# Performance work log

Hardware: AMD Instinct MI355X
Metric: run time of the kernel (lower is better)

## Reference

```python
import jax, jax.numpy as jnp
import numpy as np

N, P, D, C = 8192, 512, 2, 4   # queries, coeff grid points, spatial dim, num coefficients
HA = 32                        # attention_net hidden
HP, CP = 32, 16                # pointswise_mlp hidden / output
HG = 256                       # green_function_net hidden


def setup_inputs() -> dict:
    key = jax.random.key(0)
    ks = jax.random.split(key, 16)
    g = lambda k, shp, s: jax.random.normal(k, shp, dtype=jnp.float32) * s
    return {
        "r": g(ks[0], (N, 2 * D), 1.0),
        "r_prime": g(ks[1], (N, 2 * D), 1.0),
        "coeff_x": g(ks[2], (P, D), 1.0),
        "coeff_y": g(ks[3], (P, C), 1.0),
        # attention_net MLP (no bias): concat(q,k)=4 -> 32 -> 32 -> 1
        "Wa1": g(ks[4], (2 * D, HA), 0.5),
        "Wa2": g(ks[5], (HA, HA), 1.0 / np.sqrt(HA)),
        "Wa3": g(ks[6], (HA, 1), 1.0 / np.sqrt(HA)),
        # pointswise_mlp: C -> 32 -> 16
        "Wp1": g(ks[7], (C, HP), 0.5), "bp1": jnp.zeros((HP,), jnp.float32),
        "Wp2": g(ks[8], (HP, CP), 1.0 / np.sqrt(HP)), "bp2": jnp.zeros((CP,), jnp.float32),
        # green_function_net: 4+4+16=24 -> 256 -> 256 -> 1 (exp at the end)
        "Wg1": g(ks[9], (2 * D + 2 * D + CP, HG), 1.0 / np.sqrt(24.0)), "bg1": jnp.zeros((HG,), jnp.float32),
        "Wg2": g(ks[10], (HG, HG), 1.0 / np.sqrt(HG)), "bg2": jnp.zeros((HG,), jnp.float32),
        "Wg3": g(ks[11], (HG, 1), 0.1 / np.sqrt(HG)), "bg3": jnp.zeros((1,), jnp.float32),
    }


def reference(r, r_prime, coeff_x, coeff_y,
              Wa1, Wa2, Wa3, Wp1, bp1, Wp2, bp2,
              Wg1, bg1, Wg2, bg2, Wg3, bg3):
    # --- CoefficientNet: pairwise MLP attention over the coefficient grid ---
    q = r[:, :D]  # (N, 2) spatial position only
    # first layer of attn MLP on concat([q, k]) split into q- and k- parts
    h = jax.nn.relu(q @ Wa1[:D][None if False else slice(None)]  # (N, HA)
                    [..., :] [..., :]  # no-op for readability
                    if False else (q @ Wa1[:D])[:, None, :] + (coeff_x @ Wa1[D:])[None, :, :])  # (N, P, HA)
    h = jax.nn.relu(h @ Wa2)                     # (N, P, HA)
    logits = (h @ Wa3)[..., 0]                   # (N, P)
    attn = jax.nn.softmax(logits, axis=-1)       # (N, P)
    attn_out = attn @ coeff_y                    # (N, C)
    c = jax.nn.relu(attn_out @ Wp1 + bp1) @ Wp2 + bp2  # (N, CP)
    # --- GreenFunctionNet ---
    x = jnp.concatenate([r, r_prime, c], axis=-1)       # (N, 24)
    g1 = jax.nn.relu(x @ Wg1 + bg1)
    g2 = jax.nn.relu(g1 @ Wg2 + bg2)
    return jnp.exp(g2 @ Wg3 + bg3)                      # (N, 1)
```

## Files before the change

### kernel.cpp

```cpp
#include <hip/hip_runtime.h>
#include <math.h>

#define N_ 8192
#define P_ 512

typedef __fp16 half8  __attribute__((ext_vector_type(8)));
typedef __fp16 half2t __attribute__((ext_vector_type(2)));
typedef float  floatx16 __attribute__((ext_vector_type(16)));

union H8 { half8 v; half2t h2[4]; };

static __device__ __forceinline__ half2t pk2(float a, float b) {
    return __builtin_amdgcn_cvt_pkrtz(a, b);
}

#define HP_OFF 17408
#define XS_OFF 21760

__global__ __launch_bounds__(512, 4) void k_fused(
    const float* __restrict__ r,
    const float* __restrict__ rp,
    const float* __restrict__ coeff_x,
    const float* __restrict__ coeff_y,
    const float* __restrict__ Wa1,
    const float* __restrict__ Wa2,
    const float* __restrict__ Wa3,
    const float* __restrict__ Wp1,
    const float* __restrict__ bp1,
    const float* __restrict__ Wp2,
    const float* __restrict__ bp2,
    const float* __restrict__ Wg1,
    const float* __restrict__ bg1,
    const float* __restrict__ Wg2,
    const float* __restrict__ bg2,
    const float* __restrict__ Wg3,
    const float* __restrict__ bg3,
    float* __restrict__ out)
{
    __shared__ __align__(16) unsigned char reg0[49152];
    __shared__ __align__(16) float4 cyS[512];
    __shared__ float sA[8][32];
    __shared__ float aoA[4][8][32];
    __shared__ float aoS[32][4];

    const int tid  = threadIdx.x;
    const int n0   = blockIdx.x * 32;
    const int lane = tid & 63;
    const int wv   = tid >> 6;
    const int j32  = lane & 31;
    const int hl   = lane >> 5;
    const int k0g  = hl * 8;

    {
        const float2 cx = ((const float2*)coeff_x)[tid];
        half2t* wrow = (half2t*)(reg0 + tid * 96);
#pragma unroll
        for (int q = 0; q < 16; ++q) {
            const float b0 = cx.x * Wa1[64 + 2*q]     + cx.y * Wa1[96 + 2*q];
            const float b1 = cx.x * Wa1[64 + 2*q + 1] + cx.y * Wa1[96 + 2*q + 1];
            wrow[q] = pk2(b0, b1);
        }
        cyS[tid] = ((const float4*)coeff_y)[tid];
    }

    H8 anh1, anh2;
    {
        const float2 rv = ((const float2*)r)[2 * (n0 + j32)];
#pragma unroll
        for (int q = 0; q < 4; ++q) {
            const int k1 = k0g + 2*q, k2 = 16 + k0g + 2*q;
            anh1.h2[q] = pk2(rv.x*Wa1[k1]   + rv.y*Wa1[32+k1],
                             rv.x*Wa1[k1+1] + rv.y*Wa1[32+k1+1]);
            anh2.h2[q] = pk2(rv.x*Wa1[k2]   + rv.y*Wa1[32+k2],
                             rv.x*Wa1[k2+1] + rv.y*Wa1[32+k2+1]);
        }
    }
    H8 af1, af2;
#pragma unroll
    for (int q = 0; q < 4; ++q) {
        af1.h2[q] = pk2(Wa2[(k0g + 2*q)     * 32 + j32],
                        Wa2[(k0g + 2*q + 1) * 32 + j32]);
        af2.h2[q] = pk2(Wa2[(16 + k0g + 2*q)     * 32 + j32],
                        Wa2[(16 + k0g + 2*q + 1) * 32 + j32]);
    }
    half2t w3h[8];
#pragma unroll
    for (int q = 0; q < 8; ++q) {
        const int r0 = ((2*q) & 3) + 8*(q >> 1) + 4*hl;
        w3h[q] = pk2(Wa3[r0], Wa3[r0 + 1]);
    }

    __syncthreads();

    const half2t zero2 = pk2(0.f, 0.f);
    float s = 0.0f, aox = 0.f, aoy = 0.f, aoz = 0.f, aow = 0.f;

#pragma unroll 2
    for (int pl = 0; pl < 64; ++pl) {
        const int ploc = wv * 64 + pl;
        const half2t* rowq = (const half2t*)(reg0 + ploc * 96) + hl * 4;

        H8 bf1, bf2;
#pragma unroll
        for (int q = 0; q < 4; ++q) {
            bf1.h2[q] = __builtin_elementwise_max(anh1.h2[q] + rowq[q],     zero2);
            bf2.h2[q] = __builtin_elementwise_max(anh2.h2[q] + rowq[8 + q], zero2);
        }

        floatx16 zc = {};
        floatx16 acc = __builtin_amdgcn_mfma_f32_32x32x16_f16(af1.v, bf1.v, zc, 0, 0, 0);
        acc = __builtin_amdgcn_mfma_f32_32x32x16_f16(af2.v, bf2.v, acc, 0, 0, 0);

        float d0, d1, d2, d3;
        {
            half2t z0 = __builtin_elementwise_max(pk2(acc[0],  acc[1]),  zero2);
            half2t z1 = __builtin_elementwise_max(pk2(acc[2],  acc[3]),  zero2);
            half2t z2 = __builtin_elementwise_max(pk2(acc[4],  acc[5]),  zero2);
            half2t z3 = __builtin_elementwise_max(pk2(acc[6],  acc[7]),  zero2);
            half2t z4 = __builtin_elementwise_max(pk2(acc[8],  acc[9]),  zero2);
            half2t z5 = __builtin_elementwise_max(pk2(acc[10], acc[11]), zero2);
            half2t z6 = __builtin_elementwise_max(pk2(acc[12], acc[13]), zero2);
            half2t z7 = __builtin_elementwise_max(pk2(acc[14], acc[15]), zero2);
            d0 = __builtin_amdgcn_fdot2(z1, w3h[1], __builtin_amdgcn_fdot2(z0, w3h[0], 0.f, false), false);
            d1 = __builtin_amdgcn_fdot2(z3, w3h[3], __builtin_amdgcn_fdot2(z2, w3h[2], 0.f, false), false);
            d2 = __builtin_amdgcn_fdot2(z5, w3h[5], __builtin_amdgcn_fdot2(z4, w3h[4], 0.f, false), false);
            d3 = __builtin_amdgcn_fdot2(z7, w3h[7], __builtin_amdgcn_fdot2(z6, w3h[6], 0.f, false), false);
        }
        float dot = (d0 + d1) + (d2 + d3);
        dot += __shfl_xor(dot, 32);

        const float e = __expf(dot);
        const float4 cyv = cyS[ploc];
        s   += e;
        aox += e * cyv.x;
        aoy += e * cyv.y;
        aoz += e * cyv.z;
        aow += e * cyv.w;
    }

    if (lane < 32) {
        sA[wv][lane]      = s;
        aoA[0][wv][lane]  = aox;
        aoA[1][wv][lane]  = aoy;
        aoA[2][wv][lane]  = aoz;
        aoA[3][wv][lane]  = aow;
    }
    __syncthreads();

    if (tid < 32) {
        float S = 0.f, A0 = 0.f, A1 = 0.f, A2 = 0.f, A3 = 0.f;
#pragma unroll
        for (int w = 0; w < 8; ++w) {
            S  += sA[w][tid];
            A0 += aoA[0][w][tid];
            A1 += aoA[1][w][tid];
            A2 += aoA[2][w][tid];
            A3 += aoA[3][w][tid];
        }
        const float inv = 1.0f / S;
        aoS[tid][0] = A0 * inv;
        aoS[tid][1] = A1 * inv;
        aoS[tid][2] = A2 * inv;
        aoS[tid][3] = A3 * inv;
    }
    __syncthreads();

    float* hpS = (float*)(reg0 + HP_OFF);
    float* xS  = (float*)(reg0 + XS_OFF);
    const int nB = tid & 31;
    const int iB = tid >> 5;

    if (tid < 256) {
        const int nn = tid >> 3, k = tid & 7;
        xS[nn*25 + k] = (k < 4) ? r[(n0+nn)*4 + k] : rp[(n0+nn)*4 + k - 4];
    }
    {
        const float a0 = aoS[nB][0], a1 = aoS[nB][1], a2 = aoS[nB][2], a3 = aoS[nB][3];
#pragma unroll
        for (int rep = 0; rep < 2; ++rep) {
            const int i = iB + rep*16;
            float a = bp1[i] + a0*Wp1[i] + a1*Wp1[32+i] + a2*Wp1[64+i] + a3*Wp1[96+i];
            hpS[nB*33 + i] = fmaxf(a, 0.0f);
        }
    }
    __syncthreads();

    {
        float a = bp2[iB];
#pragma unroll
        for (int i = 0; i < 32; ++i) a += hpS[nB*33 + i] * Wp2[i*16 + iB];
        xS[nB*25 + 8 + iB] = a;
    }
    __syncthreads();

    const int jcol = (wv << 5) + j32;
    __fp16* g1S = (__fp16*)reg0;

    {
        H8 xa1, xa2, wb1, wb2;
        const float* xrow = xS + j32 * 25;
#pragma unroll
        for (int q = 0; q < 4; ++q) {
            xa1.h2[q] = pk2(xrow[k0g + 2*q], xrow[k0g + 2*q + 1]);
            wb1.h2[q] = pk2(Wg1[(k0g + 2*q)*256 + jcol],
                            Wg1[(k0g + 2*q + 1)*256 + jcol]);
            if (hl == 0) {
                xa2.h2[q] = pk2(xrow[16 + 2*q], xrow[16 + 2*q + 1]);
                wb2.h2[q] = pk2(Wg1[(16 + 2*q)*256 + jcol],
                                Wg1[(17 + 2*q)*256 + jcol]);
            } else {
                xa2.h2[q] = pk2(0.f, 0.f);
                wb2.h2[q] = pk2(0.f, 0.f);
            }
        }
        floatx16 g1acc = {};
        g1acc = __builtin_amdgcn_mfma_f32_32x32x16_f16(xa1.v, wb1.v, g1acc, 0, 0, 0);
        g1acc = __builtin_amdgcn_mfma_f32_32x32x16_f16(xa2.v, wb2.v, g1acc, 0, 0, 0);

        const float b1v = bg1[jcol];
#pragma unroll
        for (int i = 0; i < 16; ++i) {
            const int row = (i & 3) + 8*(i >> 2) + 4*hl;
            g1S[row*264 + jcol] = (__fp16)fmaxf(g1acc[i] + b1v, 0.0f);
        }
    }
    __syncthreads();

    {
        floatx16 acc2 = {};
        const __fp16* arow = g1S + j32 * 264;

        H8 wB[4], wBn[4];
#pragma unroll
        for (int q = 0; q < 4; ++q) {
            const int kb = q*16 + hl*8;
#pragma unroll
            for (int t = 0; t < 4; ++t)
                wB[q].h2[t] = pk2(Wg2[(kb + 2*t)*256 + jcol],
                                  Wg2[(kb + 2*t + 1)*256 + jcol]);
        }
#pragma unroll
        for (int c = 0; c < 4; ++c) {
            if (c < 3) {
#pragma unroll
                for (int q = 0; q < 4; ++q) {
                    const int kb = (c*4 + 4 + q)*16 + hl*8;
#pragma unroll
                    for (int t = 0; t < 4; ++t)
                        wBn[q].h2[t] = pk2(Wg2[(kb + 2*t)*256 + jcol],
                                           Wg2[(kb + 2*t + 1)*256 + jcol]);
                }
            }
#pragma unroll
            for (int q = 0; q < 4; ++q) {
                H8 af;
                af.v = *(const half8*)(arow + (c*4 + q)*16 + hl*8);
                acc2 = __builtin_amdgcn_mfma_f32_32x32x16_f16(af.v, wB[q].v, acc2, 0, 0, 0);
            }
#pragma unroll
            for (int q = 0; q < 4; ++q) wB[q] = wBn[q];
        }

        const float b2v = bg2[jcol];
        const float w3v = Wg3[jcol];
        float part[16];
#pragma unroll
        for (int i = 0; i < 16; ++i)
            part[i] = fmaxf(acc2[i] + b2v, 0.0f) * w3v;
#pragma unroll
        for (int off = 1; off <= 16; off <<= 1) {
#pragma unroll
            for (int i = 0; i < 16; ++i) part[i] += __shfl_xor(part[i], off);
        }
        float* redS = &sA[0][0];
        if ((lane & 31) == 0) {
#pragma unroll
            for (int i = 0; i < 16; ++i) {
                const int row = (i & 3) + 8*(i >> 2) + 4*hl;
                redS[wv*32 + row] = part[i];
            }
        }
        __syncthreads();

        if (tid < 32) {
            float v = bg3[0];
#pragma unroll
            for (int w = 0; w < 8; ++w) v += redS[w*32 + tid];
            out[n0 + tid] = __expf(v);
        }
    }
}

extern "C" void kernel_launch(void* const* d_in, const int* in_sizes, int n_in,
                              void* d_out, int out_size, void* d_ws, size_t ws_size,
                              hipStream_t stream)
{
    const float* r   = (const float*)d_in[0];
    const float* rp  = (const float*)d_in[1];
    const float* cx  = (const float*)d_in[2];
    const float* cy  = (const float*)d_in[3];
    const float* Wa1 = (const float*)d_in[4];
    const float* Wa2 = (const float*)d_in[5];
    const float* Wa3 = (const float*)d_in[6];
    const float* Wp1 = (const float*)d_in[7];
    const float* bp1 = (const float*)d_in[8];
    const float* Wp2 = (const float*)d_in[9];
    const float* bp2 = (const float*)d_in[10];
    const float* Wg1 = (const float*)d_in[11];
    const float* bg1 = (const float*)d_in[12];
    const float* Wg2 = (const float*)d_in[13];
    const float* bg2 = (const float*)d_in[14];
    const float* Wg3 = (const float*)d_in[15];
    const float* bg3 = (const float*)d_in[16];

    hipLaunchKernelGGL(k_fused, dim3(N_/32), dim3(512), 0, stream,
                       r, rp, cx, cy, Wa1, Wa2, Wa3, Wp1, bp1, Wp2, bp2,
                       Wg1, bg1, Wg2, bg2, Wg3, bg3, (float*)d_out);
}
```

Before: 110.2 us.

## Double block to 1024 threads, splitting attention loop and Wg2 GEMM split-K

Raises the workgroup size from 512 to 1024 threads. Each of the 16 waves now handles 32 coefficient points in the attention loop instead of 64. The 256x256 green-function layer is split along K across two wave groups, and the partial accumulators are summed through shared memory. With only 256 blocks on the device, this is meant to put more waves on each CU to hide latency. In exchange it adds LDS traffic and an extra barrier, and may increase register pressure under the new launch bounds.

```diff
diff --git a/kernel.cpp b/kernel.cpp
--- a/kernel.cpp
+++ b/kernel.cpp
@@ -16,8 +16,9 @@
 
 #define HP_OFF 17408
 #define XS_OFF 21760
-
-__global__ __launch_bounds__(512, 4) void k_fused(
+#define PC_OFF 18944
+
+__global__ __launch_bounds__(1024, 4) void k_fused(
     const float* __restrict__ r,
     const float* __restrict__ rp,
     const float* __restrict__ coeff_x,
@@ -37,10 +38,10 @@
     const float* __restrict__ bg3,
     float* __restrict__ out)
 {
-    __shared__ __align__(16) unsigned char reg0[49152];
+    __shared__ __align__(16) unsigned char reg0[52224];
     __shared__ __align__(16) float4 cyS[512];
-    __shared__ float sA[8][32];
-    __shared__ float aoA[4][8][32];
+    __shared__ float sA[16][32];
+    __shared__ float aoA[4][16][32];
     __shared__ float aoS[32][4];
 
     const int tid  = threadIdx.x;
@@ -51,7 +52,7 @@
     const int hl   = lane >> 5;
     const int k0g  = hl * 8;
 
-    {
+    if (tid < 512) {
         const float2 cx = ((const float2*)coeff_x)[tid];
         half2t* wrow = (half2t*)(reg0 + tid * 96);
 #pragma unroll
@@ -60,7 +61,8 @@
             const float b1 = cx.x * Wa1[64 + 2*q + 1] + cx.y * Wa1[96 + 2*q + 1];
             wrow[q] = pk2(b0, b1);
         }
-        cyS[tid] = ((const float4*)coeff_y)[tid];
+    } else {
+        cyS[tid - 512] = ((const float4*)coeff_y)[tid - 512];
     }
 
     H8 anh1, anh2;
@@ -96,8 +98,8 @@
     float s = 0.0f, aox = 0.f, aoy = 0.f, aoz = 0.f, aow = 0.f;
 
 #pragma unroll 2
-    for (int pl = 0; pl < 64; ++pl) {
-        const int ploc = wv * 64 + pl;
+    for (int pl = 0; pl < 32; ++pl) {
+        const int ploc = wv * 32 + pl;
         const half2t* rowq = (const half2t*)(reg0 + ploc * 96) + hl * 4;
 
         H8 bf1, bf2;
@@ -150,7 +152,7 @@
     if (tid < 32) {
         float S = 0.f, A0 = 0.f, A1 = 0.f, A2 = 0.f, A3 = 0.f;
 #pragma unroll
-        for (int w = 0; w < 8; ++w) {
+        for (int w = 0; w < 16; ++w) {
             S  += sA[w][tid];
             A0 += aoA[0][w][tid];
             A1 += aoA[1][w][tid];
@@ -168,13 +170,13 @@
     float* hpS = (float*)(reg0 + HP_OFF);
     float* xS  = (float*)(reg0 + XS_OFF);
     const int nB = tid & 31;
-    const int iB = tid >> 5;
+    const int iB = (tid >> 5) & 15;
 
     if (tid < 256) {
         const int nn = tid >> 3, k = tid & 7;
         xS[nn*25 + k] = (k < 4) ? r[(n0+nn)*4 + k] : rp[(n0+nn)*4 + k - 4];
     }
-    {
+    if (tid < 512) {
         const float a0 = aoS[nB][0], a1 = aoS[nB][1], a2 = aoS[nB][2], a3 = aoS[nB][3];
 #pragma unroll
         for (int rep = 0; rep < 2; ++rep) {
@@ -185,7 +187,7 @@
     }
     __syncthreads();
 
-    {
+    if (tid < 512) {
         float a = bp2[iB];
 #pragma unroll
         for (int i = 0; i < 32; ++i) a += hpS[nB*33 + i] * Wp2[i*16 + iB];
@@ -193,10 +195,10 @@
     }
     __syncthreads();
 
-    const int jcol = (wv << 5) + j32;
     __fp16* g1S = (__fp16*)reg0;
 
-    {
+    if (wv < 8) {
+        const int jcol = (wv << 5) + j32;
         H8 xa1, xa2, wb1, wb2;
         const float* xrow = xS + j32 * 25;
 #pragma unroll
@@ -227,63 +229,64 @@
     __syncthreads();
 
     {
+        const int w8    = wv & 7;
+        const int khalf = wv >> 3;
+        const int jcol  = (w8 << 5) + j32;
+
         floatx16 acc2 = {};
         const __fp16* arow = g1S + j32 * 264;
-
-        H8 wB[4], wBn[4];
-#pragma unroll
-        for (int q = 0; q < 4; ++q) {
-            const int kb = q*16 + hl*8;
-#pragma unroll
-            for (int t = 0; t < 4; ++t)
-                wB[q].h2[t] = pk2(Wg2[(kb + 2*t)*256 + jcol],
-                                  Wg2[(kb + 2*t + 1)*256 + jcol]);
-        }
-#pragma unroll
-        for (int c = 0; c < 4; ++c) {
-            if (c < 3) {
-#pragma unroll
-                for (int q = 0; q < 4; ++q) {
-                    const int kb = (c*4 + 4 + q)*16 + hl*8;
-#pragma unroll
-                    for (int t = 0; t < 4; ++t)
-                        wBn[q].h2[t] = pk2(Wg2[(kb + 2*t)*256 + jcol],
-                                           Wg2[(kb + 2*t + 1)*256 + jcol]);
-                }
+#pragma unroll
+        for (int c = 0; c < 2; ++c) {
+            H8 wB[4];
+#pragma unroll
+            for (int q = 0; q < 4; ++q) {
+                const int kb = (khalf*8 + c*4 + q)*16 + hl*8;
+#pragma unroll
+                for (int t = 0; t < 4; ++t)
+                    wB[q].h2[t] = pk2(Wg2[(kb + 2*t)*256 + jcol],
+                                      Wg2[(kb + 2*t + 1)*256 + jcol]);
             }
 #pragma unroll
             for (int q = 0; q < 4; ++q) {
                 H8 af;
-                af.v = *(const half8*)(arow + (c*4 + q)*16 + hl*8);
+                af.v = *(const half8*)(arow + (khalf*8 + c*4 + q)*16 + hl*8);
                 acc2 = __builtin_amdgcn_mfma_f32_32x32x16_f16(af.v, wB[q].v, acc2, 0, 0, 0);
             }
-#pragma unroll
-            for (int q = 0; q < 4; ++q) wB[q] = wBn[q];
-        }
-
-        const float b2v = bg2[jcol];
-        const float w3v = Wg3[jcol];
-        float part[16];
-#pragma unroll
-        for (int i = 0; i < 16; ++i)
-            part[i] = fmaxf(acc2[i] + b2v, 0.0f) * w3v;
-#pragma unroll
-        for (int off = 1; off <= 16; off <<= 1) {
-#pragma unroll
-            for (int i = 0; i < 16; ++i) part[i] += __shfl_xor(part[i], off);
-        }
-        float* redS = &sA[0][0];
-        if ((lane & 31) == 0) {
-#pragma unroll
-            for (int i = 0; i < 16; ++i) {
-                const int row = (i & 3) + 8*(i >> 2) + 4*hl;
-                redS[wv*32 + row] = part[i];
+        }
+
+        float* pc = (float*)(reg0 + PC_OFF) + w8 * 1024;
+        if (khalf == 1) {
+#pragma unroll
+            for (int i = 0; i < 16; ++i) pc[i*64 + lane] = acc2[i];
+        }
+        __syncthreads();
+
+        if (khalf == 0) {
+            const float b2v = bg2[jcol];
+            const float w3v = Wg3[jcol];
+            float part[16];
+#pragma unroll
+            for (int i = 0; i < 16; ++i)
+                part[i] = fmaxf(acc2[i] + pc[i*64 + lane] + b2v, 0.0f) * w3v;
+#pragma unroll
+            for (int off = 1; off <= 16; off <<= 1) {
+#pragma unroll
+                for (int i = 0; i < 16; ++i) part[i] += __shfl_xor(part[i], off);
+            }
+            float* redS = &sA[0][0];
+            if ((lane & 31) == 0) {
+#pragma unroll
+                for (int i = 0; i < 16; ++i) {
+                    const int row = (i & 3) + 8*(i >> 2) + 4*hl;
+                    redS[w8*32 + row] = part[i];
+                }
             }
         }
         __syncthreads();
 
         if (tid < 32) {
             float v = bg3[0];
+            float* redS = &sA[0][0];
 #pragma unroll
             for (int w = 0; w < 8; ++w) v += redS[w*32 + tid];
             out[n0 + tid] = __expf(v);
@@ -313,7 +316,7 @@
     const float* Wg3 = (const float*)d_in[15];
     const float* bg3 = (const float*)d_in[16];
 
-    hipLaunchKernelGGL(k_fused, dim3(N_/32), dim3(512), 0, stream,
+    hipLaunchKernelGGL(k_fused, dim3(N_/32), dim3(1024), 0, stream,
                        r, rp, cx, cy, Wa1, Wa2, Wa3, Wp1, bp1, Wp2, bp2,
                        Wg1, bg1, Wg2, bg2, Wg3, bg3, (float*)d_out);
 }
```

After: 110.4 us. No clear change (+0.2%).
